# Kernel optimization log

Measured on AMD Instinct MI355X. Metric: run time of the kernel, lower is better.

The kernel has to match this reference:

```python
import jax, jax.numpy as jnp
import numpy as np

NUM_RELATIONS = 8


def rgcn_conv(x, edge_index, edge_type, W, root, bias):
    """PyG RGCNConv (full weights, aggr='mean'): for each relation r, mean-aggregate
    W_r @ x_src over incoming edges of type r at each target node, sum over relations,
    then add root transform and bias."""
    N = x.shape[0]
    src, dst = edge_index[0], edge_index[1]
    # per-(relation, dst) edge counts for mean aggregation
    comb = edge_type * N + dst  # [E]
    cnt = jax.ops.segment_sum(jnp.ones(src.shape[0], x.dtype), comb,
                              num_segments=NUM_RELATIONS * N)  # [R*N]
    inv = jnp.where(cnt > 0, 1.0 / cnt, 0.0)
    # per-relation transformed features [R, N, H]
    xW = jnp.einsum('ni,rio->rno', x, W)
    # per-edge message, pre-scaled by 1/count for mean aggregation
    msg = xW[edge_type, src] * inv[comb][:, None]  # [E, H]
    agg = jax.ops.segment_sum(msg, dst, num_segments=N)  # [N, H]
    return agg + x @ root + bias


def setup_inputs() -> dict:
    key = jax.random.key(0)
    ks = jax.random.split(key, 9)
    N, E, D, H, C, R = 50000, 600000, 128, 128, 16, NUM_RELATIONS
    s1 = 1.0 / np.sqrt(D)
    s2 = 1.0 / np.sqrt(H)
    return {
        'x': jax.random.normal(ks[0], (N, D), jnp.float32),
        'edge_index': jax.random.randint(ks[1], (2, E), 0, N, jnp.int32),
        'edge_type': jax.random.randint(ks[2], (E,), 0, R, jnp.int32),
        'W1': jax.random.normal(ks[3], (R, D, H), jnp.float32) * s1,
        'root1': jax.random.normal(ks[4], (D, H), jnp.float32) * s1,
        'b1': jnp.zeros((H,), jnp.float32),
        'W2': jax.random.normal(ks[5], (R, H, H), jnp.float32) * s2,
        'root2': jax.random.normal(ks[6], (H, H), jnp.float32) * s2,
        'b2': jnp.zeros((H,), jnp.float32),
        'Wc': jax.random.normal(ks[7], (H, C), jnp.float32) * s2,
        'bc': jnp.zeros((C,), jnp.float32),
    }


def reference(x, edge_index, edge_type, W1, root1, b1, W2, root2, b2, Wc, bc):
    h = jax.nn.relu(rgcn_conv(x, edge_index, edge_type, W1, root1, b1))
    # dropout(p=0.2) is identity in eval mode
    embeddings = rgcn_conv(h, edge_index, edge_type, W2, root2, b2)
    out = embeddings @ Wc + bc
    return (out, embeddings)
```

## Files before the change

### kernel.cpp

```cpp
#include <hip/hip_runtime.h>

#define NREL 8

typedef __attribute__((ext_vector_type(8))) short bf16x8;
typedef __attribute__((ext_vector_type(4))) float f32x4;

__device__ inline ushort f2bf(float f)
{
    union { float f; unsigned u; } v; v.f = f;
    unsigned r = v.u + 0x7FFF + ((v.u >> 16) & 1);
    return (ushort)(r >> 16);
}

__device__ inline unsigned cvtpk(float lo, float hi)
{
    unsigned r;
    asm("v_cvt_pk_bf16_f32 %0, %1, %2" : "=v"(r) : "v"(lo), "v"(hi));
    return r;
}

__global__ __launch_bounds__(256) void zero16(float4* __restrict__ p, int n4)
{
    int i = blockIdx.x * 256 + threadIdx.x;
    int stride = gridDim.x * 256;
    for (; i < n4; i += stride) p[i] = make_float4(0.f, 0.f, 0.f, 0.f);
}

__global__ __launch_bounds__(256) void count_edges(
    const int* __restrict__ ei, const int* __restrict__ et,
    int* __restrict__ cnt, int E, int N)
{
    int e = blockIdx.x * 256 + threadIdx.x;
    if (e < E) {
        int d = ei[E + e];
        int r = et[e];
        atomicAdd(&cnt[r * N + d], 1);
    }
}

__global__ __launch_bounds__(256) void scan1f(
    const int* __restrict__ cnt, float* __restrict__ invc8,
    int* __restrict__ part, int* __restrict__ bsum, int N)
{
    __shared__ int tmp[256];
    int d = blockIdx.x * 256 + threadIdx.x;
    int s = 0;
    if (d < N) {
        #pragma unroll
        for (int r = 0; r < NREL; r++) {
            int c = cnt[r * N + d];
            s += c;
            invc8[(size_t)d * 8 + r] = (c > 0) ? 1.f / (float)c : 0.f;
        }
    }
    int v = s;
    tmp[threadIdx.x] = v;
    __syncthreads();
    for (int off = 1; off < 256; off <<= 1) {
        int t = (threadIdx.x >= off) ? tmp[threadIdx.x - off] : 0;
        __syncthreads();
        tmp[threadIdx.x] += t;
        __syncthreads();
    }
    if (d < N) part[d] = tmp[threadIdx.x] - v;
    if (threadIdx.x == 255) bsum[blockIdx.x] = tmp[255];
}

__global__ __launch_bounds__(1024) void scan2(int* __restrict__ bsum, int nb)
{
    __shared__ int tmp[1024];
    int tid = threadIdx.x;
    int v = (tid < nb) ? bsum[tid] : 0;
    tmp[tid] = v;
    __syncthreads();
    for (int off = 1; off < 1024; off <<= 1) {
        int t = (tid >= off) ? tmp[tid - off] : 0;
        __syncthreads();
        tmp[tid] += t;
        __syncthreads();
    }
    if (tid < nb) bsum[tid] = tmp[tid] - v;
}

__global__ __launch_bounds__(256) void scan3(
    const int* __restrict__ part, const int* __restrict__ bsum,
    int* __restrict__ rowptr, int* __restrict__ cursor, int n, int E)
{
    int i = blockIdx.x * 256 + threadIdx.x;
    if (i < n) {
        int v = part[i] + bsum[blockIdx.x];
        rowptr[i] = v;
        cursor[i] = v;
    }
    if (i == 0) rowptr[n] = E;
}

__global__ __launch_bounds__(256) void fill_csr(
    const int* __restrict__ ei, const int* __restrict__ et,
    int* __restrict__ cursor, int* __restrict__ spk, int E)
{
    int e = blockIdx.x * 256 + threadIdx.x;
    if (e < E) {
        int d = ei[E + e];
        int pos = atomicAdd(&cursor[d], 1);
        spk[pos] = (ei[e] << 8) | et[e];
    }
}

__global__ __launch_bounds__(256) void conv_x(
    const float* __restrict__ x, ushort* __restrict__ xb, int n4)
{
    int i = blockIdx.x * 256 + threadIdx.x;
    int stride = gridDim.x * 256;
    for (; i < n4; i += stride) {
        float4 v = ((const float4*)x)[i];
        ushort4 o;
        o.x = f2bf(v.x); o.y = f2bf(v.y); o.z = f2bf(v.z); o.w = f2bf(v.w);
        ((ushort4*)xb)[i] = o;
    }
}

__global__ __launch_bounds__(256) void conv_wfB(
    const float* __restrict__ W1, const float* __restrict__ root1,
    ushort* __restrict__ Wf1,
    const float* __restrict__ W2, const float* __restrict__ root2,
    ushort* __restrict__ Wf2)
{
    const float* W    = blockIdx.y ? W2 : W1;
    const float* root = blockIdx.y ? root2 : root1;
    ushort* Wf        = blockIdx.y ? Wf2 : Wf1;
    int i = blockIdx.x * 256 + threadIdx.x;
    if (i >= 128 * 1152) return;
    int f = i >> 9;
    int within = i & 511;
    int l = within >> 3;
    int j = within & 7;
    int rs = f >> 5;
    int kk = (f >> 3) & 3;
    int n  = f & 7;
    int col = (n << 4) | (l & 15);
    int kl  = kk * 32 + (l >> 4) * 8 + j;
    float v = (rs < 8) ? W[rs * 16384 + kl * 128 + col] : root[kl * 128 + col];
    Wf[i] = f2bf(v);
}

__global__ __launch_bounds__(1024) void fused_layer(
    const ushort* __restrict__ Xb, const int* __restrict__ rowptr,
    const int* __restrict__ spk, const float* __restrict__ invc8,
    const ushort* __restrict__ Wf, const float* __restrict__ bias,
    float* __restrict__ Ofp, ushort* __restrict__ Obf,
    const float* __restrict__ Wc, const float* __restrict__ bc,
    float* __restrict__ outC, int N, int relu)
{
    __shared__ ushort lds[8 * 16 * 128];
    __shared__ f32x4 pscr[8 * 64];
    __shared__ float wcs[128][16];
    __shared__ float bcs[16];
    __shared__ float embt[16][128];

    int wid  = threadIdx.x >> 6;
    int lane = threadIdx.x & 63;
    int blk0 = blockIdx.x * 16;
    int lane4 = lane << 2;

    if (outC) {
        for (int i = threadIdx.x; i < 2048; i += 1024)
            wcs[i >> 4][i & 15] = Wc[i];
        if (threadIdx.x < 16) bcs[threadIdx.x] = bc[threadIdx.x];
    }

    {
        int lrow16 = wid;
        int d = blk0 + lrow16;

        float2 a0 = {0.f, 0.f}, a1 = {0.f, 0.f}, a2 = {0.f, 0.f}, a3 = {0.f, 0.f};
        float2 a4 = {0.f, 0.f}, a5 = {0.f, 0.f}, a6 = {0.f, 0.f}, a7 = {0.f, 0.f};

        #define ROWLD(SP) \
            (*(const unsigned*)((const char*)Xb + (unsigned)((SP) | lane4)))
        #define CONSUME(P, U)                                               \
        {                                                                   \
            union { unsigned u; float f; } lo, hi;                          \
            lo.u = (U) << 16; hi.u = (U) & 0xFFFF0000u;                     \
            switch ((P) & 0xFF) {                                           \
                case 0: a0.x += lo.f; a0.y += hi.f; break;                  \
                case 1: a1.x += lo.f; a1.y += hi.f; break;                  \
                case 2: a2.x += lo.f; a2.y += hi.f; break;                  \
                case 3: a3.x += lo.f; a3.y += hi.f; break;                  \
                case 4: a4.x += lo.f; a4.y += hi.f; break;                  \
                case 5: a5.x += lo.f; a5.y += hi.f; break;                  \
                case 6: a6.x += lo.f; a6.y += hi.f; break;                  \
                default: a7.x += lo.f; a7.y += hi.f; break;                 \
            }                                                               \
        }

        if (d < N) {
            int beg = rowptr[d], end = rowptr[d + 1];
            int i = beg;
            for (; i + 8 <= end; i += 8) {
                int pk8 = spk[i + (lane & 7)];
                int p0 = __builtin_amdgcn_readlane(pk8, 0);
                int p1 = __builtin_amdgcn_readlane(pk8, 1);
                int p2 = __builtin_amdgcn_readlane(pk8, 2);
                int p3 = __builtin_amdgcn_readlane(pk8, 3);
                int p4 = __builtin_amdgcn_readlane(pk8, 4);
                int p5 = __builtin_amdgcn_readlane(pk8, 5);
                int p6 = __builtin_amdgcn_readlane(pk8, 6);
                int p7 = __builtin_amdgcn_readlane(pk8, 7);
                unsigned u0 = ROWLD(p0 & 0xFFFFFF00);
                unsigned u1 = ROWLD(p1 & 0xFFFFFF00);
                unsigned u2 = ROWLD(p2 & 0xFFFFFF00);
                unsigned u3 = ROWLD(p3 & 0xFFFFFF00);
                unsigned u4 = ROWLD(p4 & 0xFFFFFF00);
                unsigned u5 = ROWLD(p5 & 0xFFFFFF00);
                unsigned u6 = ROWLD(p6 & 0xFFFFFF00);
                unsigned u7 = ROWLD(p7 & 0xFFFFFF00);
                CONSUME(p0, u0);
                CONSUME(p1, u1);
                CONSUME(p2, u2);
                CONSUME(p3, u3);
                CONSUME(p4, u4);
                CONSUME(p5, u5);
                CONSUME(p6, u6);
                CONSUME(p7, u7);
            }
            for (; i + 4 <= end; i += 4) {
                int pk4 = spk[i + (lane & 3)];
                int p0 = __builtin_amdgcn_readlane(pk4, 0);
                int p1 = __builtin_amdgcn_readlane(pk4, 1);
                int p2 = __builtin_amdgcn_readlane(pk4, 2);
                int p3 = __builtin_amdgcn_readlane(pk4, 3);
                unsigned u0 = ROWLD(p0 & 0xFFFFFF00);
                unsigned u1 = ROWLD(p1 & 0xFFFFFF00);
                unsigned u2 = ROWLD(p2 & 0xFFFFFF00);
                unsigned u3 = ROWLD(p3 & 0xFFFFFF00);
                CONSUME(p0, u0);
                CONSUME(p1, u1);
                CONSUME(p2, u2);
                CONSUME(p3, u3);
            }
            for (; i < end; i++) {
                int p = __builtin_amdgcn_readfirstlane(spk[i]);
                unsigned u = ROWLD(p & 0xFFFFFF00);
                CONSUME(p, u);
            }
        }
        #undef CONSUME
        #undef ROWLD

        f32x4 iv0 = {0.f, 0.f, 0.f, 0.f}, iv1 = {0.f, 0.f, 0.f, 0.f};
        if (d < N) {
            iv0 = *(const f32x4*)&invc8[(size_t)d * 8];
            iv1 = *(const f32x4*)&invc8[(size_t)d * 8 + 4];
        }
        unsigned swz = (unsigned)(lrow16 & 7) << 4;
        char* rowbase = (char*)lds + (lrow16 << 8);
        unsigned wroff = (((unsigned)lane << 2)) ^ swz;
        #define WR2(R, A, IV)                                               \
        {                                                                   \
            unsigned pk = cvtpk(A.x * (IV), A.y * (IV));                    \
            *(unsigned*)(rowbase + (R << 12) + wroff) = pk;                 \
        }
        WR2(0, a0, iv0[0]) WR2(1, a1, iv0[1]) WR2(2, a2, iv0[2]) WR2(3, a3, iv0[3])
        WR2(4, a4, iv1[0]) WR2(5, a5, iv1[1]) WR2(6, a6, iv1[2]) WR2(7, a7, iv1[3])
        #undef WR2
    }
    __syncthreads();

    int lrow = lane & 15;
    int kgrp = lane >> 4;
    unsigned swzR = (unsigned)(lrow & 7) << 4;
    const bf16x8* Wf8 = (const bf16x8*)Wf;
    int n0    = wid & 7;
    int upper = wid >> 3;

    f32x4 acc = {0.f, 0.f, 0.f, 0.f};
    const char* abase = (const char*)lds + (lrow << 8);

    int rs0 = upper * 4;
    #pragma unroll 1
    for (int rs = rs0; rs < rs0 + 4; rs++) {
        const bf16x8* Bp = Wf8 + (size_t)rs * 2048 + (size_t)n0 * 64 + lane;
        const char* ab = abase + (rs << 12);
        bf16x8 a0 = *(const bf16x8*)(ab + ((unsigned)(0 * 64 + kgrp * 16) ^ swzR));
        bf16x8 a1 = *(const bf16x8*)(ab + ((unsigned)(1 * 64 + kgrp * 16) ^ swzR));
        bf16x8 a2 = *(const bf16x8*)(ab + ((unsigned)(2 * 64 + kgrp * 16) ^ swzR));
        bf16x8 a3 = *(const bf16x8*)(ab + ((unsigned)(3 * 64 + kgrp * 16) ^ swzR));
        bf16x8 b0 = Bp[0];
        bf16x8 b1 = Bp[512];
        bf16x8 b2 = Bp[1024];
        bf16x8 b3 = Bp[1536];
        acc = __builtin_amdgcn_mfma_f32_16x16x32_bf16(a0, b0, acc, 0, 0, 0);
        acc = __builtin_amdgcn_mfma_f32_16x16x32_bf16(a1, b1, acc, 0, 0, 0);
        acc = __builtin_amdgcn_mfma_f32_16x16x32_bf16(a2, b2, acc, 0, 0, 0);
        acc = __builtin_amdgcn_mfma_f32_16x16x32_bf16(a3, b3, acc, 0, 0, 0);
    }
    {
        int arow = blk0 + lrow; if (arow >= N) arow = N - 1;
        const ushort* A = Xb + (size_t)arow * 128;
        const bf16x8* Bp = Wf8 + (size_t)8 * 2048 + (size_t)n0 * 64 + lane;
        int kkb = upper * 2;
        bf16x8 a0 = *(const bf16x8*)(A + (kkb + 0) * 32 + kgrp * 8);
        bf16x8 a1 = *(const bf16x8*)(A + (kkb + 1) * 32 + kgrp * 8);
        bf16x8 b0 = Bp[(kkb + 0) * 512];
        bf16x8 b1 = Bp[(kkb + 1) * 512];
        acc = __builtin_amdgcn_mfma_f32_16x16x32_bf16(a0, b0, acc, 0, 0, 0);
        acc = __builtin_amdgcn_mfma_f32_16x16x32_bf16(a1, b1, acc, 0, 0, 0);
    }

    if (upper) pscr[(size_t)n0 * 64 + lane] = acc;
    __syncthreads();

    if (!upper) {
        f32x4 po = pscr[(size_t)n0 * 64 + lane];
        int row0 = blk0 + kgrp * 4;
        int col  = n0 * 16 + lrow;
        float bv = bias[col];
        #pragma unroll
        for (int r = 0; r < 4; r++) {
            int row = row0 + r;
            float v = acc[r] + po[r] + bv;
            if (relu) v = fmaxf(v, 0.f);
            if (outC) embt[kgrp * 4 + r][col] = v;
            if (row < N) {
                if (Ofp) Ofp[(size_t)row * 128 + col] = v;
                if (Obf) Obf[(size_t)row * 128 + col] = f2bf(v);
            }
        }
    }

    if (outC) {
        __syncthreads();
        if (lane < 16) {
            float acc2 = bcs[lane];
            const float* er = embt[wid];
            #pragma unroll 8
            for (int k = 0; k < 128; k++) acc2 += er[k] * wcs[k][lane];
            int row = blk0 + wid;
            if (row < N) outC[(size_t)row * 16 + lane] = acc2;
        }
    }
}

static inline size_t align256(size_t x) { return (x + 255) & ~(size_t)255; }

extern "C" void kernel_launch(void* const* d_in, const int* in_sizes, int n_in,
                              void* d_out, int out_size, void* d_ws, size_t ws_size,
                              hipStream_t stream)
{
    const float* x     = (const float*)d_in[0];
    const int*   ei    = (const int*)d_in[1];
    const int*   et    = (const int*)d_in[2];
    const float* W1    = (const float*)d_in[3];
    const float* root1 = (const float*)d_in[4];
    const float* b1    = (const float*)d_in[5];
    const float* W2    = (const float*)d_in[6];
    const float* root2 = (const float*)d_in[7];
    const float* b2    = (const float*)d_in[8];
    const float* Wc    = (const float*)d_in[9];
    const float* bc    = (const float*)d_in[10];

    const int N = in_sizes[0] / 128;
    const int E = in_sizes[2];
    const int C = in_sizes[10];

    float* out = (float*)d_out;
    float* emb = out + (size_t)N * C;

    size_t cntB  = align256((size_t)NREL * N * sizeof(int));
    size_t rpB   = align256((size_t)(N + 1) * sizeof(int));
    size_t curB  = align256((size_t)N * sizeof(int));
    size_t bsB   = align256((size_t)1024 * sizeof(int));
    size_t invB  = align256((size_t)N * 8 * sizeof(float));
    size_t spkB  = align256((size_t)E * sizeof(int));
    size_t xbB   = align256((size_t)N * 128 * sizeof(ushort));
    size_t wtB   = align256((size_t)128 * 1152 * sizeof(ushort));

    char* p = (char*)d_ws;
    int*    cnt    = (int*)p;      p += cntB;
    int*    rowptr = (int*)p;      p += rpB;
    int*    cursor = (int*)p;      p += curB;
    int*    part   = (int*)p;      p += curB;
    int*    bsum   = (int*)p;      p += bsB;
    float*  invc8  = (float*)p;    p += invB;
    int*    spk    = (int*)p;      p += spkB;
    ushort* xb     = (ushort*)p;   p += xbB;
    ushort* hb     = (ushort*)p;   p += xbB;
    ushort* Wf1    = (ushort*)p;   p += wtB;
    ushort* Wf2    = (ushort*)p;

    dim3 blk(256);
    int gE    = (E + 255) / 256;
    int gN    = (N + 255) / 256;
    int gFus  = (N + 15) / 16;
    int gWt   = (128 * 1152 + 255) / 256;
    long long cnt4 = (long long)NREL * N / 4;
    int gZ = (int)((cnt4 + 255) / 256); if (gZ > 2048) gZ = 2048;
    int nx4 = N * 32;
    int gCx = (nx4 + 255) / 256; if (gCx > 2048) gCx = 2048;

    zero16<<<gZ, blk, 0, stream>>>((float4*)cnt, (int)cnt4);
    count_edges<<<gE, blk, 0, stream>>>(ei, et, cnt, E, N);
    scan1f<<<gN, blk, 0, stream>>>(cnt, invc8, part, bsum, N);
    scan2<<<1, 1024, 0, stream>>>(bsum, gN);
    scan3<<<gN, blk, 0, stream>>>(part, bsum, rowptr, cursor, N, E);
    fill_csr<<<gE, blk, 0, stream>>>(ei, et, cursor, spk, E);

    conv_x<<<gCx, blk, 0, stream>>>(x, xb, nx4);
    conv_wfB<<<dim3(gWt, 2), blk, 0, stream>>>(W1, root1, Wf1, W2, root2, Wf2);

    fused_layer<<<gFus, dim3(1024), 0, stream>>>(
        xb, rowptr, spk, invc8, Wf1, b1, nullptr, hb,
        nullptr, nullptr, nullptr, N, 1);

    fused_layer<<<gFus, dim3(1024), 0, stream>>>(
        hb, rowptr, spk, invc8, Wf2, b2, emb, nullptr,
        Wc, bc, out, N, 0);
}
```

Baseline: 271.8 us.

## Process 32 rows per fused block and split classifier into separate kernel

Result: faster. 261.1 us (-4.0%).

```diff
diff --git a/kernel.cpp b/kernel.cpp
--- a/kernel.cpp
+++ b/kernel.cpp
@@ -144,34 +144,24 @@
     Wf[i] = f2bf(v);
 }
 
-__global__ __launch_bounds__(1024) void fused_layer(
+__global__ __launch_bounds__(1024, 8) void fused_layer(
     const ushort* __restrict__ Xb, const int* __restrict__ rowptr,
     const int* __restrict__ spk, const float* __restrict__ invc8,
     const ushort* __restrict__ Wf, const float* __restrict__ bias,
-    float* __restrict__ Ofp, ushort* __restrict__ Obf,
-    const float* __restrict__ Wc, const float* __restrict__ bc,
-    float* __restrict__ outC, int N, int relu)
-{
-    __shared__ ushort lds[8 * 16 * 128];
-    __shared__ f32x4 pscr[8 * 64];
-    __shared__ float wcs[128][16];
-    __shared__ float bcs[16];
-    __shared__ float embt[16][128];
+    float* __restrict__ Ofp, ushort* __restrict__ Obf, int N, int relu)
+{
+    __shared__ ushort lds[8 * 32 * 128];
+    __shared__ f32x4 pscr[2][512];
 
     int wid  = threadIdx.x >> 6;
     int lane = threadIdx.x & 63;
-    int blk0 = blockIdx.x * 16;
+    int blk0 = blockIdx.x * 32;
     int lane4 = lane << 2;
 
-    if (outC) {
-        for (int i = threadIdx.x; i < 2048; i += 1024)
-            wcs[i >> 4][i & 15] = Wc[i];
-        if (threadIdx.x < 16) bcs[threadIdx.x] = bc[threadIdx.x];
-    }
-
-    {
-        int lrow16 = wid;
-        int d = blk0 + lrow16;
+    #pragma unroll 1
+    for (int rr = 0; rr < 2; rr++) {
+        int lrow32 = wid * 2 + rr;
+        int d = blk0 + lrow32;
 
         float2 a0 = {0.f, 0.f}, a1 = {0.f, 0.f}, a2 = {0.f, 0.f}, a3 = {0.f, 0.f};
         float2 a4 = {0.f, 0.f}, a5 = {0.f, 0.f}, a6 = {0.f, 0.f}, a7 = {0.f, 0.f};
@@ -253,13 +243,13 @@
             iv0 = *(const f32x4*)&invc8[(size_t)d * 8];
             iv1 = *(const f32x4*)&invc8[(size_t)d * 8 + 4];
         }
-        unsigned swz = (unsigned)(lrow16 & 7) << 4;
-        char* rowbase = (char*)lds + (lrow16 << 8);
+        unsigned swz = (unsigned)(lrow32 & 7) << 4;
+        char* rowbase = (char*)lds + (lrow32 << 8);
         unsigned wroff = (((unsigned)lane << 2)) ^ swz;
         #define WR2(R, A, IV)                                               \
         {                                                                   \
             unsigned pk = cvtpk(A.x * (IV), A.y * (IV));                    \
-            *(unsigned*)(rowbase + (R << 12) + wroff) = pk;                 \
+            *(unsigned*)(rowbase + (R << 13) + wroff) = pk;                 \
         }
         WR2(0, a0, iv0[0]) WR2(1, a1, iv0[1]) WR2(2, a2, iv0[2]) WR2(3, a3, iv0[3])
         WR2(4, a4, iv1[0]) WR2(5, a5, iv1[1]) WR2(6, a6, iv1[2]) WR2(7, a7, iv1[3])
@@ -274,72 +264,103 @@
     int n0    = wid & 7;
     int upper = wid >> 3;
 
-    f32x4 acc = {0.f, 0.f, 0.f, 0.f};
-    const char* abase = (const char*)lds + (lrow << 8);
+    f32x4 acc0 = {0.f, 0.f, 0.f, 0.f};
+    f32x4 acc1 = {0.f, 0.f, 0.f, 0.f};
+    const char* ldsb = (const char*)lds;
 
     int rs0 = upper * 4;
     #pragma unroll 1
     for (int rs = rs0; rs < rs0 + 4; rs++) {
         const bf16x8* Bp = Wf8 + (size_t)rs * 2048 + (size_t)n0 * 64 + lane;
-        const char* ab = abase + (rs << 12);
-        bf16x8 a0 = *(const bf16x8*)(ab + ((unsigned)(0 * 64 + kgrp * 16) ^ swzR));
-        bf16x8 a1 = *(const bf16x8*)(ab + ((unsigned)(1 * 64 + kgrp * 16) ^ swzR));
-        bf16x8 a2 = *(const bf16x8*)(ab + ((unsigned)(2 * 64 + kgrp * 16) ^ swzR));
-        bf16x8 a3 = *(const bf16x8*)(ab + ((unsigned)(3 * 64 + kgrp * 16) ^ swzR));
         bf16x8 b0 = Bp[0];
         bf16x8 b1 = Bp[512];
         bf16x8 b2 = Bp[1024];
         bf16x8 b3 = Bp[1536];
-        acc = __builtin_amdgcn_mfma_f32_16x16x32_bf16(a0, b0, acc, 0, 0, 0);
-        acc = __builtin_amdgcn_mfma_f32_16x16x32_bf16(a1, b1, acc, 0, 0, 0);
-        acc = __builtin_amdgcn_mfma_f32_16x16x32_bf16(a2, b2, acc, 0, 0, 0);
-        acc = __builtin_amdgcn_mfma_f32_16x16x32_bf16(a3, b3, acc, 0, 0, 0);
+        const char* ab0 = ldsb + (rs << 13) + ((0 + lrow) << 8);
+        const char* ab1 = ldsb + (rs << 13) + ((16 + lrow) << 8);
+        {
+            bf16x8 a0 = *(const bf16x8*)(ab0 + ((unsigned)(0 * 64 + kgrp * 16) ^ swzR));
+            bf16x8 a1 = *(const bf16x8*)(ab0 + ((unsigned)(1 * 64 + kgrp * 16) ^ swzR));
+            bf16x8 a2 = *(const bf16x8*)(ab0 + ((unsigned)(2 * 64 + kgrp * 16) ^ swzR));
+            bf16x8 a3 = *(const bf16x8*)(ab0 + ((unsigned)(3 * 64 + kgrp * 16) ^ swzR));
+            acc0 = __builtin_amdgcn_mfma_f32_16x16x32_bf16(a0, b0, acc0, 0, 0, 0);
+            acc0 = __builtin_amdgcn_mfma_f32_16x16x32_bf16(a1, b1, acc0, 0, 0, 0);
+            acc0 = __builtin_amdgcn_mfma_f32_16x16x32_bf16(a2, b2, acc0, 0, 0, 0);
+            acc0 = __builtin_amdgcn_mfma_f32_16x16x32_bf16(a3, b3, acc0, 0, 0, 0);
+        }
+        {
+            bf16x8 a0 = *(const bf16x8*)(ab1 + ((unsigned)(0 * 64 + kgrp * 16) ^ swzR));
+            bf16x8 a1 = *(const bf16x8*)(ab1 + ((unsigned)(1 * 64 + kgrp * 16) ^ swzR));
+            bf16x8 a2 = *(const bf16x8*)(ab1 + ((unsigned)(2 * 64 + kgrp * 16) ^ swzR));
+            bf16x8 a3 = *(const bf16x8*)(ab1 + ((unsigned)(3 * 64 + kgrp * 16) ^ swzR));
+            acc1 = __builtin_amdgcn_mfma_f32_16x16x32_bf16(a0, b0, acc1, 0, 0, 0);
+            acc1 = __builtin_amdgcn_mfma_f32_16x16x32_bf16(a1, b1, acc1, 0, 0, 0);
+            acc1 = __builtin_amdgcn_mfma_f32_16x16x32_bf16(a2, b2, acc1, 0, 0, 0);
+            acc1 = __builtin_amdgcn_mfma_f32_16x16x32_bf16(a3, b3, acc1, 0, 0, 0);
+        }
     }
     {
-        int arow = blk0 + lrow; if (arow >= N) arow = N - 1;
-        const ushort* A = Xb + (size_t)arow * 128;
+        int arow0 = blk0 + lrow;      if (arow0 >= N) arow0 = N - 1;
+        int arow1 = blk0 + 16 + lrow; if (arow1 >= N) arow1 = N - 1;
+        const ushort* A0 = Xb + (size_t)arow0 * 128;
+        const ushort* A1 = Xb + (size_t)arow1 * 128;
         const bf16x8* Bp = Wf8 + (size_t)8 * 2048 + (size_t)n0 * 64 + lane;
         int kkb = upper * 2;
-        bf16x8 a0 = *(const bf16x8*)(A + (kkb + 0) * 32 + kgrp * 8);
-        bf16x8 a1 = *(const bf16x8*)(A + (kkb + 1) * 32 + kgrp * 8);
         bf16x8 b0 = Bp[(kkb + 0) * 512];
         bf16x8 b1 = Bp[(kkb + 1) * 512];
-        acc = __builtin_amdgcn_mfma_f32_16x16x32_bf16(a0, b0, acc, 0, 0, 0);
-        acc = __builtin_amdgcn_mfma_f32_16x16x32_bf16(a1, b1, acc, 0, 0, 0);
-    }
-
-    if (upper) pscr[(size_t)n0 * 64 + lane] = acc;
+        bf16x8 a00 = *(const bf16x8*)(A0 + (kkb + 0) * 32 + kgrp * 8);
+        bf16x8 a01 = *(const bf16x8*)(A0 + (kkb + 1) * 32 + kgrp * 8);
+        bf16x8 a10 = *(const bf16x8*)(A1 + (kkb + 0) * 32 + kgrp * 8);
+        bf16x8 a11 = *(const bf16x8*)(A1 + (kkb + 1) * 32 + kgrp * 8);
+        acc0 = __builtin_amdgcn_mfma_f32_16x16x32_bf16(a00, b0, acc0, 0, 0, 0);
+        acc0 = __builtin_amdgcn_mfma_f32_16x16x32_bf16(a01, b1, acc0, 0, 0, 0);
+        acc1 = __builtin_amdgcn_mfma_f32_16x16x32_bf16(a10, b0, acc1, 0, 0, 0);
+        acc1 = __builtin_amdgcn_mfma_f32_16x16x32_bf16(a11, b1, acc1, 0, 0, 0);
+    }
+
+    if (upper) {
+        pscr[0][n0 * 64 + lane] = acc0;
+        pscr[1][n0 * 64 + lane] = acc1;
+    }
     __syncthreads();
 
     if (!upper) {
-        f32x4 po = pscr[(size_t)n0 * 64 + lane];
-        int row0 = blk0 + kgrp * 4;
-        int col  = n0 * 16 + lrow;
+        f32x4 p0 = pscr[0][n0 * 64 + lane];
+        f32x4 p1 = pscr[1][n0 * 64 + lane];
+        int col = n0 * 16 + lrow;
         float bv = bias[col];
         #pragma unroll
-        for (int r = 0; r < 4; r++) {
-            int row = row0 + r;
-            float v = acc[r] + po[r] + bv;
-            if (relu) v = fmaxf(v, 0.f);
-            if (outC) embt[kgrp * 4 + r][col] = v;
-            if (row < N) {
-                if (Ofp) Ofp[(size_t)row * 128 + col] = v;
-                if (Obf) Obf[(size_t)row * 128 + col] = f2bf(v);
+        for (int rg = 0; rg < 2; rg++) {
+            int row0 = blk0 + rg * 16 + kgrp * 4;
+            f32x4 a = rg ? acc1 : acc0;
+            f32x4 pp = rg ? p1 : p0;
+            #pragma unroll
+            for (int r = 0; r < 4; r++) {
+                int row = row0 + r;
+                if (row < N) {
+                    float v = a[r] + pp[r] + bv;
+                    if (relu) v = fmaxf(v, 0.f);
+                    if (Ofp) Ofp[(size_t)row * 128 + col] = v;
+                    if (Obf) Obf[(size_t)row * 128 + col] = f2bf(v);
+                }
             }
         }
     }
-
-    if (outC) {
-        __syncthreads();
-        if (lane < 16) {
-            float acc2 = bcs[lane];
-            const float* er = embt[wid];
-            #pragma unroll 8
-            for (int k = 0; k < 128; k++) acc2 += er[k] * wcs[k][lane];
-            int row = blk0 + wid;
-            if (row < N) outC[(size_t)row * 16 + lane] = acc2;
-        }
-    }
+}
+
+__global__ __launch_bounds__(256) void classifier(
+    const float* __restrict__ emb, const float* __restrict__ Wc,
+    const float* __restrict__ bc, float* __restrict__ out, int N)
+{
+    int t = threadIdx.x;
+    int c = t & 15;
+    int n = blockIdx.x * 16 + (t >> 4);
+    if (n >= N) return;
+    const float* e = emb + (size_t)n * 128;
+    float acc = bc[c];
+    #pragma unroll 8
+    for (int k = 0; k < 128; k++) acc += e[k] * Wc[k * 16 + c];
+    out[(size_t)n * 16 + c] = acc;
 }
 
 static inline size_t align256(size_t x) { return (x + 255) & ~(size_t)255; }
@@ -392,7 +413,8 @@
     dim3 blk(256);
     int gE    = (E + 255) / 256;
     int gN    = (N + 255) / 256;
-    int gFus  = (N + 15) / 16;
+    int gFus  = (N + 31) / 32;
+    int gCls  = (N + 15) / 16;
     int gWt   = (128 * 1152 + 255) / 256;
     long long cnt4 = (long long)NREL * N / 4;
     int gZ = (int)((cnt4 + 255) / 256); if (gZ > 2048) gZ = 2048;
@@ -410,10 +432,10 @@
     conv_wfB<<<dim3(gWt, 2), blk, 0, stream>>>(W1, root1, Wf1, W2, root2, Wf2);
 
     fused_layer<<<gFus, dim3(1024), 0, stream>>>(
-        xb, rowptr, spk, invc8, Wf1, b1, nullptr, hb,
-        nullptr, nullptr, nullptr, N, 1);
+        xb, rowptr, spk, invc8, Wf1, b1, nullptr, hb, N, 1);
 
     fused_layer<<<gFus, dim3(1024), 0, stream>>>(
-        hb, rowptr, spk, invc8, Wf2, b2, emb, nullptr,
-        Wc, bc, out, N, 0);
-}
+        hb, rowptr, spk, invc8, Wf2, b2, emb, nullptr, N, 0);
+
+    classifier<<<gCls, blk, 0, stream>>>(emb, Wc, bc, out, N);
+}
```
